# Kernel tuning notes

Measured on AMD Instinct MI355X. Metric: run time of the kernel, lower is better.

## Reference

```python
import jax, jax.numpy as jnp
import numpy as np

B, C, H, W = 128, 3, 256, 256
STEPS = 64
T_MIN, T_MAX = 0.02, 0.98
RES = (T_MAX - T_MIN) / (STEPS - 1)


def setup_inputs() -> dict:
    key = jax.random.key(0)
    x = jax.random.uniform(key, (B, C, H, W), dtype=jnp.float32)
    return {"x": x}


def _cell_filtrations(V):
    # V-construction cubical complex (sublevel): vertex cells carry pixel values,
    # edge cells carry max of their 2 endpoint vertices, square cells max of 4 corners.
    Eh = jnp.maximum(V[..., :, :-1], V[..., :, 1:])          # [.., H,   W-1] horizontal edges (dim 1)
    Ev = jnp.maximum(V[..., :-1, :], V[..., 1:, :])          # [.., H-1, W  ] vertical edges (dim 1)
    S = jnp.maximum(jnp.maximum(V[..., :-1, :-1], V[..., :-1, 1:]),
                    jnp.maximum(V[..., 1:, :-1], V[..., 1:, 1:]))  # [.., H-1, W-1] squares (dim 2)
    return Eh, Ev, S


def _bins(f):
    # t = max(ceil((filt - t_min)/resolution), 0); cells with filt > t_max are masked out.
    return jnp.clip(jnp.ceil((f - T_MIN) / RES).astype(jnp.int32), 0, STEPS - 1)


def reference(x):
    b, c = x.shape[0], x.shape[1]
    V = x  # sublevel filtration
    Eh, Ev, S = _cell_filtrations(V)
    filts = jnp.concatenate([V.reshape(b, c, -1), Eh.reshape(b, c, -1),
                             Ev.reshape(b, c, -1), S.reshape(b, c, -1)], axis=-1)
    n_v = H * W
    n_eh = H * (W - 1)
    n_ev = (H - 1) * W
    n_s = (H - 1) * (W - 1)
    # Euler characteristic signs (-1)**dim per cell type.
    signs = jnp.concatenate([jnp.ones(n_v, jnp.float32), -jnp.ones(n_eh, jnp.float32),
                             -jnp.ones(n_ev, jnp.float32), jnp.ones(n_s, jnp.float32)])
    t = _bins(filts)                                   # [B, C, N] bin index per cell
    contrib = signs * (filts <= T_MAX).astype(jnp.float32)

    def one_image(tb, cb):
        ecc = jnp.zeros(STEPS, jnp.float32).at[tb].add(cb)
        return jnp.cumsum(ecc)

    return jax.vmap(jax.vmap(one_image))(t, contrib)   # [B, C, STEPS]
```

## Files before the change

kernel.cpp:

```cpp
#include <hip/hip_runtime.h>

#define IMG     256
#define NIMG    384
#define STEPS   64
#define ROWS_PT 32
#define STRIPS  4
#define ROWS_PB (ROWS_PT * STRIPS)
#define BANDS   (IMG / ROWS_PB)
#define INFV    1e30f

__device__ __forceinline__ int bin_of(float v) {
    int t = (int)ceilf(__builtin_fmaf(v, 65.625f, -1.3125f));
    t = t < 0 ? 0 : t;
    return t > 63 ? 63 : t;
}

__device__ __forceinline__ void load_row(const float* __restrict__ base,
                                         int r, int col0, float w[6]) {
    if ((unsigned)r >= IMG) {
        w[0] = w[1] = w[2] = w[3] = w[4] = w[5] = INFV;
        return;
    }
    const float* p = base + r * IMG + col0;
    float4 q = *(const float4*)p;
    w[1] = q.x; w[2] = q.y; w[3] = q.z; w[4] = q.w;
    w[0] = (col0 > 0)       ? p[-1] : INFV;
    w[5] = (col0 + 4 < IMG) ? p[4]  : INFV;
}

__global__ __launch_bounds__(256) void ecc_main(const float* __restrict__ x,
                                                int* __restrict__ hist) {
    const int img   = blockIdx.x / BANDS;
    const int band  = blockIdx.x % BANDS;
    const int lane  = threadIdx.x & 63;
    const int strip = threadIdx.x >> 6;
    const int col0  = lane * 4;
    const int r0    = band * ROWS_PB + strip * ROWS_PT;

    __shared__ int lh[STRIPS][STEPS];
    ((int*)lh)[threadIdx.x] = 0;
    __syncthreads();

    const float* base = x + (size_t)img * (IMG * IMG);

    float u[6], c[6], d[6], n[6];
    load_row(base, r0 - 1, col0, u);
    load_row(base, r0,     col0, c);
    load_row(base, r0 + 1, col0, d);

    for (int k = 0; k < ROWS_PT; ++k) {
        load_row(base, r0 + k + 2, col0, n);
#pragma unroll
        for (int i = 1; i <= 4; ++i) {
            float cv = c[i];
            if (cv <= 0.98f) {
                bool oR = (c[i + 1] <  cv);
                bool oL = (c[i - 1] <= cv);
                bool oD = (d[i]     <  cv);
                bool oU = (u[i]     <= cv);
                bool sDR = oR & oD & (d[i + 1] <  cv);
                bool sDL = oL & oD & (d[i - 1] <  cv);
                bool sUR = oU & oR & (u[i + 1] <= cv);
                bool sUL = oU & oL & (u[i - 1] <= cv);
                int contrib = 1 - ((int)oR + (int)oL + (int)oD + (int)oU)
                                + ((int)sDR + (int)sDL + (int)sUR + (int)sUL);
                if (contrib) atomicAdd(&lh[strip][bin_of(cv)], contrib);
            }
        }
#pragma unroll
        for (int i = 0; i < 6; ++i) { u[i] = c[i]; c[i] = d[i]; d[i] = n[i]; }
    }

    __syncthreads();
    if (threadIdx.x < STEPS) {
        int t = threadIdx.x;
        hist[blockIdx.x * STEPS + t] = lh[0][t] + lh[1][t] + lh[2][t] + lh[3][t];
    }
}

__global__ __launch_bounds__(64) void ecc_scan(const int* __restrict__ hist,
                                               float* __restrict__ out) {
    const int img = blockIdx.x;
    const int t   = threadIdx.x;
    int v = hist[(img * BANDS + 0) * STEPS + t] + hist[(img * BANDS + 1) * STEPS + t];
#pragma unroll
    for (int s = 1; s < 64; s <<= 1) {
        int y = __shfl_up(v, s, 64);
        if (t >= s) v += y;
    }
    out[img * STEPS + t] = (float)v;
}

extern "C" void kernel_launch(void* const* d_in, const int* in_sizes, int n_in,
                              void* d_out, int out_size, void* d_ws, size_t ws_size,
                              hipStream_t stream) {
    const float* x = (const float*)d_in[0];
    float* out = (float*)d_out;
    int* hist = (int*)d_ws;

    ecc_main<<<dim3(NIMG * BANDS), dim3(256), 0, stream>>>(x, hist);
    ecc_scan<<<dim3(NIMG), dim3(64), 0, stream>>>(hist, out);
}
```

Baseline: 163.9 us.

## Shrink rows per wave, fetch halo via shuffles, fully unroll row loop

Each wave now processes 8 rows instead of 32, which gives 8 bands per image and four times as many blocks, so more of the GPU is busy at once. The left and right halo pixels are taken from neighbouring lanes with cross-lane shuffles instead of extra scalar global loads. The row loop is fully unrolled, and the scan kernel now sums over all bands. In exchange, each wave reloads more overlapping halo rows, and more partial histograms have to be written and then reduced.

```diff
diff --git a/kernel.cpp b/kernel.cpp
--- a/kernel.cpp
+++ b/kernel.cpp
@@ -3,9 +3,9 @@
 #define IMG     256
 #define NIMG    384
 #define STEPS   64
-#define ROWS_PT 32
-#define STRIPS  4
-#define ROWS_PB (ROWS_PT * STRIPS)
+#define ROWS_PW 8
+#define WAVES   4
+#define ROWS_PB (ROWS_PW * WAVES)
 #define BANDS   (IMG / ROWS_PB)
 #define INFV    1e30f
 
@@ -15,41 +15,40 @@
     return t > 63 ? 63 : t;
 }
 
-__device__ __forceinline__ void load_row(const float* __restrict__ base,
-                                         int r, int col0, float w[6]) {
-    if ((unsigned)r >= IMG) {
-        w[0] = w[1] = w[2] = w[3] = w[4] = w[5] = INFV;
-        return;
-    }
-    const float* p = base + r * IMG + col0;
-    float4 q = *(const float4*)p;
-    w[1] = q.x; w[2] = q.y; w[3] = q.z; w[4] = q.w;
-    w[0] = (col0 > 0)       ? p[-1] : INFV;
-    w[5] = (col0 + 4 < IMG) ? p[4]  : INFV;
-}
-
 __global__ __launch_bounds__(256) void ecc_main(const float* __restrict__ x,
                                                 int* __restrict__ hist) {
-    const int img   = blockIdx.x / BANDS;
-    const int band  = blockIdx.x % BANDS;
-    const int lane  = threadIdx.x & 63;
-    const int strip = threadIdx.x >> 6;
-    const int col0  = lane * 4;
-    const int r0    = band * ROWS_PB + strip * ROWS_PT;
+    const int img  = blockIdx.x / BANDS;
+    const int band = blockIdx.x % BANDS;
+    const int lane = threadIdx.x & 63;
+    const int wave = threadIdx.x >> 6;
+    const int col0 = lane * 4;
+    const int r0   = band * ROWS_PB + wave * ROWS_PW;
 
-    __shared__ int lh[STRIPS][STEPS];
+    __shared__ int lh[WAVES][STEPS];
     ((int*)lh)[threadIdx.x] = 0;
     __syncthreads();
 
     const float* base = x + (size_t)img * (IMG * IMG);
 
+    auto load6 = [&](int r, float w[6]) {
+        float4 q;
+        if ((unsigned)r < IMG) q = *(const float4*)(base + r * IMG + col0);
+        else                   q = make_float4(INFV, INFV, INFV, INFV);
+        w[1] = q.x; w[2] = q.y; w[3] = q.z; w[4] = q.w;
+        float left  = __shfl_up(q.w, 1, 64);
+        float right = __shfl_down(q.x, 1, 64);
+        w[0] = (lane == 0)  ? INFV : left;
+        w[5] = (lane == 63) ? INFV : right;
+    };
+
     float u[6], c[6], d[6], n[6];
-    load_row(base, r0 - 1, col0, u);
-    load_row(base, r0,     col0, c);
-    load_row(base, r0 + 1, col0, d);
+    load6(r0 - 1, u);
+    load6(r0,     c);
+    load6(r0 + 1, d);
 
-    for (int k = 0; k < ROWS_PT; ++k) {
-        load_row(base, r0 + k + 2, col0, n);
+#pragma unroll
+    for (int k = 0; k < ROWS_PW; ++k) {
+        load6(r0 + k + 2, n);
 #pragma unroll
         for (int i = 1; i <= 4; ++i) {
             float cv = c[i];
@@ -64,7 +63,7 @@
                 bool sUL = oU & oL & (u[i - 1] <= cv);
                 int contrib = 1 - ((int)oR + (int)oL + (int)oD + (int)oU)
                                 + ((int)sDR + (int)sDL + (int)sUR + (int)sUL);
-                if (contrib) atomicAdd(&lh[strip][bin_of(cv)], contrib);
+                if (contrib) atomicAdd(&lh[wave][bin_of(cv)], contrib);
             }
         }
 #pragma unroll
@@ -82,7 +81,10 @@
                                                float* __restrict__ out) {
     const int img = blockIdx.x;
     const int t   = threadIdx.x;
-    int v = hist[(img * BANDS + 0) * STEPS + t] + hist[(img * BANDS + 1) * STEPS + t];
+    int v = 0;
+#pragma unroll
+    for (int b = 0; b < BANDS; ++b)
+        v += hist[(img * BANDS + b) * STEPS + t];
 #pragma unroll
     for (int s = 1; s < 64; s <<= 1) {
         int y = __shfl_up(v, s, 64);
```

Result: faster. 153.9 us (-6.1%).
